# Kernel optimization log

Hardware: AMD Instinct MI355X
Metric: run time of the kernel (lower is better)

The kernel has to match this reference:

```python
import jax, jax.numpy as jnp
import numpy as np

B, C, T = 4, 512, 4096


def setup_inputs() -> dict:
    key = jax.random.key(0)
    ks = jax.random.split(key, 9)
    s = 1.0 / np.sqrt(C)
    return {
        "x": jax.random.normal(ks[0], (B, C, T), jnp.float32),
        "Wq": jax.random.normal(ks[1], (C, C), jnp.float32) * s,
        "bq": jax.random.normal(ks[2], (C,), jnp.float32) * 0.01,
        "Wk": jax.random.normal(ks[3], (C, C), jnp.float32) * s,
        "bk": jax.random.normal(ks[4], (C,), jnp.float32) * 0.01,
        "Wv": jax.random.normal(ks[5], (C, C), jnp.float32) * s,
        "bv": jax.random.normal(ks[6], (C,), jnp.float32) * 0.01,
        "Wp": jax.random.normal(ks[7], (C, C), jnp.float32) * s,
        "bp": jax.random.normal(ks[8], (C,), jnp.float32) * 0.01,
    }


def reference(x, Wq, bq, Wk, bk, Wv, bv, Wp, bp):
    # x: [B, C, T]; kernel-size-1 causal convs == pointwise linears over channels.
    b, c, t = x.shape
    q = jnp.einsum('oc,bct->bto', Wq, x) + bq  # [B, T, C]
    k = jnp.einsum('oc,bct->bto', Wk, x) + bk
    v = jnp.einsum('oc,bct->bto', Wv, x) + bv
    scale = jnp.asarray(c, x.dtype) ** -0.5
    w = jnp.einsum('btc,bsc->bts', q, k) * scale  # [B, T, T]
    mask = jnp.tril(jnp.ones((t, t), bool))        # causal: query t attends s<=t
    w = jnp.where(mask, w, -jnp.inf)
    w = jax.nn.softmax(w, axis=-1)
    h = jnp.einsum('bts,bsc->btc', w, v)           # [B, T, C]
    out = jnp.einsum('oc,btc->bot', Wp, h) + bp[None, :, None]  # [B, C, T]
    return x + out
```

## Files before the change

### kernel.cpp

```cpp
#include <hip/hip_runtime.h>

#define NB 4
#define NC 512
#define NT 4096
#define NTILE 528

typedef __attribute__((ext_vector_type(4))) float f32x4;
typedef __attribute__((ext_vector_type(8))) short short8;

typedef const __attribute__((address_space(1))) unsigned int* gp1_t;
typedef __attribute__((address_space(3))) unsigned int* lp3_t;

__device__ __forceinline__ void gload16(const short* g, short* l) {
  __builtin_amdgcn_global_load_lds((gp1_t)g, (lp3_t)l, 16, 0, 0);
}

#define BARRIER()  asm volatile("s_barrier" ::: "memory")
#define WAITVM0()  asm volatile("s_waitcnt vmcnt(0)" ::: "memory")
#define WAITVM4()  asm volatile("s_waitcnt vmcnt(4)" ::: "memory")
#define WAITVM8()  asm volatile("s_waitcnt vmcnt(8)" ::: "memory")
#define WAITVM12() asm volatile("s_waitcnt vmcnt(12)" ::: "memory")
#define WAITVM16() asm volatile("s_waitcnt vmcnt(16)" ::: "memory")

__device__ __forceinline__ short f2bf(float f) {
  union { float f; unsigned u; } v; v.f = f;
  unsigned r = v.u + 0x7fffu + ((v.u >> 16) & 1u);
  return (short)(r >> 16);
}
__device__ __forceinline__ float bf2f(short s) {
  union { unsigned u; float f; } v; v.u = ((unsigned)(unsigned short)s) << 16;
  return v.f;
}

#define SCOL_SWZ(lane) ((((lane) & 3) ^ (((lane) >> 3) & 3)) * 8)
#define FKO_SWZ(lane)  (((((lane) >> 4) ^ (((lane) >> 1) & 3)) & 3) * 8)

template <int NBUF>
__device__ __forceinline__ void gemm_tile(const short* __restrict__ A, int lda,
                                          const short* __restrict__ Bg, int ldb,
                                          int m0, int n0, int ksteps,
                                          f32x4 (&acc)[4][4], short* lds) {
  const int tid  = threadIdx.x;
  const int lane = tid & 63;
  const int wv   = tid >> 6;
  const int wm = (wv >> 1) * 64;
  const int wn = (wv & 1) * 64;
  const int srow = wv * 16 + (lane >> 2);
  const int scol = SCOL_SWZ(lane);
  const int fm  = lane & 15;
  const int fko = FKO_SWZ(lane);

  const short* Ap0 = A  + (size_t)(m0 + srow) * lda + scol;
  const short* Ap1 = Ap0 + (size_t)64 * lda;
  const short* Bp0 = Bg + (size_t)(n0 + srow) * ldb + scol;
  const short* Bp1 = Bp0 + (size_t)64 * ldb;

  auto issue = [&](int kt) {
    short* base = lds + (kt % NBUF) * 8192;
    const int k0 = kt * 32;
    gload16(Ap0 + k0, base + wv * 512);
    gload16(Ap1 + k0, base + 2048 + wv * 512);
    gload16(Bp0 + k0, base + 4096 + wv * 512);
    gload16(Bp1 + k0, base + 6144 + wv * 512);
  };

  issue(0);
#pragma unroll
  for (int p = 1; p < NBUF - 1; ++p)
    if (p < ksteps) issue(p);

  for (int kt = 0; kt < ksteps; ++kt) {
    const short* As = lds + (kt % NBUF) * 8192;
    const short* Bs = As + 4096;
    if (kt) BARRIER();
    if constexpr (NBUF == 5) {
      if (kt + 4 < ksteps)      { issue(kt + 4); WAITVM16(); }
      else if (kt + 3 < ksteps) { WAITVM12(); }
      else if (kt + 2 < ksteps) { WAITVM8(); }
      else if (kt + 1 < ksteps) { WAITVM4(); }
      else                      { WAITVM0(); }
    } else {
      if (kt + 2 < ksteps)      { issue(kt + 2); WAITVM8(); }
      else if (kt + 1 < ksteps) { WAITVM4(); }
      else                      { WAITVM0(); }
    }
    BARRIER();
    short8 af[4], bfr[4];
#pragma unroll
    for (int i = 0; i < 4; ++i)
      af[i] = *(const short8*)(As + (wm + i * 16 + fm) * 32 + fko);
#pragma unroll
    for (int j = 0; j < 4; ++j)
      bfr[j] = *(const short8*)(Bs + (wn + j * 16 + fm) * 32 + fko);
#pragma unroll
    for (int i = 0; i < 4; ++i)
#pragma unroll
      for (int j = 0; j < 4; ++j)
        acc[i][j] = __builtin_amdgcn_mfma_f32_16x16x32_bf16(af[i], bfr[j], acc[i][j], 0, 0, 0);
  }
}

#define ACC_INIT                                  \
  f32x4 acc[4][4];                                \
  {                                               \
    const f32x4 z = {0.f, 0.f, 0.f, 0.f};         \
    for (int i = 0; i < 4; ++i)                   \
      for (int j = 0; j < 4; ++j) acc[i][j] = z;  \
  }

#define EPI_IDX                                   \
  const int lane = threadIdx.x & 63;              \
  const int wave = threadIdx.x >> 6;              \
  const int wm = (wave >> 1) * 64;                \
  const int wn = (wave & 1) * 64;

#define GEMM_LDS3 __shared__ short lds[24576];
#define GEMM_LDS5 __shared__ short lds[40960];

__device__ __forceinline__ void xcd_rowchunk(int x, int nrows, int& row, int& chunk) {
  const int xcd  = x & 7;
  const int slot = x >> 3;
  row   = nrows - 1 - (xcd + 8 * (slot >> 2));
  chunk = slot & 3;
}

__device__ __forceinline__ void pv_rowchunk(int x, int z, int& bm, int& chunk) {
  const int xcd  = x & 7;
  const int slot = x >> 3;
  int ridx = slot >> 2;
  if (z >= 2) ridx = 3 - ridx;
  bm = (ridx == 0) ? (31 - xcd)
     : (ridx == 1) ? (23 - xcd)
     : (ridx == 2) ? (8 + xcd)
                   : xcd;
  chunk = slot & 3;
}

__global__ __launch_bounds__(256) void k_transpose(const float* __restrict__ x,
                                                   short* __restrict__ xT) {
  __shared__ float tile[32][33];
  const int b  = blockIdx.z;
  const int t0 = blockIdx.x * 32;
  const int c0 = blockIdx.y * 32;
  const int tx = threadIdx.x & 31;
  const int ty = threadIdx.x >> 5;
  const float* xp = x + ((size_t)b * NC + c0) * NT + t0;
#pragma unroll
  for (int i = 0; i < 32; i += 8)
    tile[ty + i][tx] = xp[(size_t)(ty + i) * NT + tx];
  __syncthreads();
  short* op = xT + ((size_t)b * NT + t0) * NC + c0;
#pragma unroll
  for (int i = 0; i < 32; i += 8)
    op[(size_t)(ty + i) * NC + tx] = f2bf(tile[tx][ty + i]);
}

__global__ __launch_bounds__(256) void k_wcvt(const float* __restrict__ s0, const float* __restrict__ s1,
                                              const float* __restrict__ s2, const float* __restrict__ s3,
                                              short* __restrict__ d0, short* __restrict__ d1,
                                              short* __restrict__ d2, short* __restrict__ d3) {
  const float* s; short* d;
  switch (blockIdx.y) {
    case 0: s = s0; d = d0; break;
    case 1: s = s1; d = d1; break;
    case 2: s = s2; d = d2; break;
    default: s = s3; d = d3; break;
  }
  const int i = (blockIdx.x * 256 + threadIdx.x) * 4;
  const float4 v = *(const float4*)(s + i);
  short4 o;
  o.x = f2bf(v.x); o.y = f2bf(v.y); o.z = f2bf(v.z); o.w = f2bf(v.w);
  *(short4*)(d + i) = o;
}

__global__ __launch_bounds__(256, 3) void k_qkv(const short* __restrict__ xT,
                                                const short* __restrict__ Wq,
                                                const float* __restrict__ bq,
                                                const short* __restrict__ Wk,
                                                const float* __restrict__ bk,
                                                const short* __restrict__ Wv,
                                                const float* __restrict__ bv,
                                                short* __restrict__ Q,
                                                short* __restrict__ K,
                                                short* __restrict__ VT) {
  GEMM_LDS3;
  const int b = blockIdx.z;
  const int y = blockIdx.y;
  int row, chunk;
  xcd_rowchunk((int)blockIdx.x, NT / 128, row, chunk);
  const short* Xb = xT + (size_t)b * NT * NC;
  ACC_INIT;
  if (y < 2) {
    const short* W = (y == 0) ? Wq : Wk;
    const float* bias = (y == 0) ? bq : bk;
    short* O = ((y == 0) ? Q : K) + (size_t)b * NT * NC;
    const int m0 = row * 128;
    const int n0 = chunk * 128;
    gemm_tile<3>(Xb, NC, W, NC, m0, n0, NC / 32, acc, lds);
    EPI_IDX;
#pragma unroll
    for (int j = 0; j < 4; ++j) {
      const int n = n0 + wn + j * 16 + (lane & 15);
      const float bv_ = bias[n];
#pragma unroll
      for (int i = 0; i < 4; ++i) {
        const int mb = m0 + wm + i * 16 + ((lane >> 4) * 4);
#pragma unroll
        for (int r = 0; r < 4; ++r)
          O[(size_t)(mb + r) * NC + n] = f2bf(acc[i][j][r] + bv_);
      }
    }
  } else {
    const int n0 = row * 128;
    const int m0 = chunk * 128;
    gemm_tile<3>(Wv, NC, Xb, NC, m0, n0, NC / 32, acc, lds);
    EPI_IDX;
    short* O = VT + (size_t)b * NC * NT;
#pragma unroll
    for (int j = 0; j < 4; ++j) {
      const int n = n0 + wn + j * 16 + (lane & 15);
#pragma unroll
      for (int i = 0; i < 4; ++i) {
        const int mb = m0 + wm + i * 16 + ((lane >> 4) * 4);
#pragma unroll
        for (int r = 0; r < 4; ++r)
          O[(size_t)(mb + r) * NT + n] = f2bf(acc[i][j][r] + bv[mb + r]);
      }
    }
  }
}

__global__ __launch_bounds__(256, 3) void k_scores(const short* __restrict__ Q,
                                                   const short* __restrict__ K,
                                                   short* __restrict__ P,
                                                   float* __restrict__ Lrow) {
  const int p = (((int)blockIdx.x & 7) * 66) + ((int)blockIdx.x >> 3);
  int bm = 0, bn = 0;
  {
    int base = 0;
    for (int sr = 0; sr < 4; ++sr) {
      bool done = false;
      for (int sc = 0; sc <= sr; ++sc) {
        const int sz = (sc == sr) ? 36 : 64;
        if (p < base + sz) {
          const int q = p - base;
          int i, j;
          if (sc == sr) {
            i = 0;
            while ((i + 1) * (i + 2) / 2 <= q) ++i;
            j = q - i * (i + 1) / 2;
          } else { i = q >> 3; j = q & 7; }
          bm = sr * 8 + i; bn = sc * 8 + j;
          done = true; break;
        }
        base += sz;
      }
      if (done) break;
    }
  }
  GEMM_LDS3;
  const int b  = blockIdx.z;
  const int m0 = bm * 128;
  const int n0 = bn * 128;
  ACC_INIT;
  gemm_tile<3>(Q + (size_t)b * NT * NC, NC, K + (size_t)b * NT * NC, NC,
               m0, n0, NC / 32, acc, lds);
  EPI_IDX;
  const float kls = 0.06376070265f;
  const int idx = bm * (bm + 1) / 2 + bn;
  short* Tp = P + ((size_t)b * NTILE + (size_t)idx) * 16384;
  float* Lp = Lrow + (size_t)b * NT;
  float psum[4][4];
#pragma unroll
  for (int i = 0; i < 4; ++i)
#pragma unroll
    for (int r = 0; r < 4; ++r) psum[i][r] = 0.f;

  if (bn < bm) {
#pragma unroll
    for (int j = 0; j < 4; ++j) {
      const int ln = wn + j * 16 + (lane & 15);
#pragma unroll
      for (int i = 0; i < 4; ++i) {
        const int lmb = wm + i * 16 + ((lane >> 4) * 4);
        const float e0 = exp2f(acc[i][j][0] * kls);
        const float e1 = exp2f(acc[i][j][1] * kls);
        const float e2 = exp2f(acc[i][j][2] * kls);
        const float e3 = exp2f(acc[i][j][3] * kls);
        unsigned pk01, pk23;
        asm("v_cvt_pk_bf16_f32 %0, %1, %2" : "=v"(pk01) : "v"(e0), "v"(e1));
        asm("v_cvt_pk_bf16_f32 %0, %1, %2" : "=v"(pk23) : "v"(e2), "v"(e3));
        Tp[(lmb + 0) * 128 + ln] = (short)(pk01 & 0xffffu);
        Tp[(lmb + 1) * 128 + ln] = (short)(pk01 >> 16);
        Tp[(lmb + 2) * 128 + ln] = (short)(pk23 & 0xffffu);
        Tp[(lmb + 3) * 128 + ln] = (short)(pk23 >> 16);
        union { unsigned u; float f; } c0, c1, c2, c3;
        c0.u = pk01 << 16; c1.u = pk01 & 0xffff0000u;
        c2.u = pk23 << 16; c3.u = pk23 & 0xffff0000u;
        psum[i][0] += c0.f; psum[i][1] += c1.f;
        psum[i][2] += c2.f; psum[i][3] += c3.f;
      }
    }
  } else {
#pragma unroll
    for (int j = 0; j < 4; ++j) {
      const int ln = wn + j * 16 + (lane & 15);
      const int n  = n0 + ln;
#pragma unroll
      for (int i = 0; i < 4; ++i) {
        const int lmb = wm + i * 16 + ((lane >> 4) * 4);
#pragma unroll
        for (int r = 0; r < 4; ++r) {
          const int m = m0 + lmb + r;
          float pr = 0.f;
          short pb = 0;
          if (n <= m) {
            pb = f2bf(exp2f(acc[i][j][r] * kls));
            pr = bf2f(pb);
          }
          Tp[(lmb + r) * 128 + ln] = pb;
          psum[i][r] += pr;
        }
      }
    }
  }
#pragma unroll
  for (int i = 0; i < 4; ++i)
#pragma unroll
    for (int r = 0; r < 4; ++r) {
      float v = psum[i][r];
      v += __shfl_xor(v, 1);
      v += __shfl_xor(v, 2);
      v += __shfl_xor(v, 4);
      v += __shfl_xor(v, 8);
      if ((lane & 15) == 0) {
        const int m = m0 + wm + i * 16 + ((lane >> 4) * 4) + r;
        atomicAdd(&Lp[m], v);
      }
    }
}

__global__ __launch_bounds__(256, 2) void k_pv(const short* __restrict__ P,
                                               const short* __restrict__ VT,
                                               const float* __restrict__ Lr,
                                               short* __restrict__ H) {
  GEMM_LDS5;
  const int b = blockIdx.z;
  int bm, chunk;
  pv_rowchunk((int)blockIdx.x, b, bm, chunk);
  const int m0 = bm * 128;
  const int n0 = chunk * 128;
  const int ksteps = (bm + 1) * 4;

  const short* Ptri = P + ((size_t)b * NTILE + (size_t)bm * (bm + 1) / 2) * 16384;
  const short* Bg   = VT + (size_t)b * NC * NT;

  ACC_INIT;
  const int tid  = threadIdx.x;
  const int lane = tid & 63;
  const int wv   = tid >> 6;
  const int wm = (wv >> 1) * 64;
  const int wn = (wv & 1) * 64;
  const int srow = wv * 16 + (lane >> 2);
  const int scol = SCOL_SWZ(lane);
  const int fm  = lane & 15;
  const int fko = FKO_SWZ(lane);

  const short* Bp0 = Bg + (size_t)(n0 + srow) * NT + scol;
  const short* Bp1 = Bp0 + (size_t)64 * NT;

  auto issue = [&](int kt) {
    short* base = lds + (kt % 5) * 8192;
    const short* At = Ptri + (size_t)(kt >> 2) * 16384 + (kt & 3) * 32;
    const short* Ap0 = At + srow * 128 + scol;
    const int k0 = kt * 32;
    gload16(Ap0, base + wv * 512);
    gload16(Ap0 + 64 * 128, base + 2048 + wv * 512);
    gload16(Bp0 + k0, base + 4096 + wv * 512);
    gload16(Bp1 + k0, base + 6144 + wv * 512);
  };

  issue(0);
#pragma unroll
  for (int p = 1; p < 4; ++p)
    if (p < ksteps) issue(p);
  for (int kt = 0; kt < ksteps; ++kt) {
    const short* As = lds + (kt % 5) * 8192;
    const short* Bs = As + 4096;
    if (kt) BARRIER();
    if (kt + 4 < ksteps)      { issue(kt + 4); WAITVM16(); }
    else if (kt + 3 < ksteps) { WAITVM12(); }
    else if (kt + 2 < ksteps) { WAITVM8(); }
    else if (kt + 1 < ksteps) { WAITVM4(); }
    else                      { WAITVM0(); }
    BARRIER();
    short8 af[4], bfr[4];
#pragma unroll
    for (int i = 0; i < 4; ++i)
      af[i] = *(const short8*)(As + (wm + i * 16 + fm) * 32 + fko);
#pragma unroll
    for (int j = 0; j < 4; ++j)
      bfr[j] = *(const short8*)(Bs + (wn + j * 16 + fm) * 32 + fko);
#pragma unroll
    for (int i = 0; i < 4; ++i)
#pragma unroll
      for (int j = 0; j < 4; ++j)
        acc[i][j] = __builtin_amdgcn_mfma_f32_16x16x32_bf16(af[i], bfr[j], acc[i][j], 0, 0, 0);
  }

  const float* L = Lr + (size_t)b * NT;
  short* Hp = H + (size_t)b * NT * NC;
#pragma unroll
  for (int i = 0; i < 4; ++i) {
    const int mb = m0 + wm + i * 16 + ((lane >> 4) * 4);
    float rinv[4];
#pragma unroll
    for (int r = 0; r < 4; ++r) rinv[r] = 1.f / L[mb + r];
#pragma unroll
    for (int j = 0; j < 4; ++j) {
      const int n = n0 + wn + j * 16 + (lane & 15);
#pragma unroll
      for (int r = 0; r < 4; ++r)
        Hp[(size_t)(mb + r) * NC + n] = f2bf(acc[i][j][r] * rinv[r]);
    }
  }
}

__global__ __launch_bounds__(256, 2) void k_out(const short* __restrict__ W,
                                                const short* __restrict__ H,
                                                const float* __restrict__ bias,
                                                const float* __restrict__ x,
                                                float* __restrict__ out) {
  GEMM_LDS5;
  const int b = blockIdx.z;
  int row, chunk;
  xcd_rowchunk((int)blockIdx.x, NT / 128, row, chunk);
  const int n0 = row * 128;
  const int m0 = chunk * 128;
  ACC_INIT;
  gemm_tile<5>(W, NC, H + (size_t)b * NT * NC, NC, m0, n0, NC / 32, acc, lds);
  EPI_IDX;
#pragma unroll
  for (int j = 0; j < 4; ++j) {
    const int n = n0 + wn + j * 16 + (lane & 15);
#pragma unroll
    for (int i = 0; i < 4; ++i) {
      const int mb = m0 + wm + i * 16 + ((lane >> 4) * 4);
#pragma unroll
      for (int r = 0; r < 4; ++r) {
        const int m = mb + r;
        const size_t idx = ((size_t)b * NC + m) * NT + n;
        out[idx] = acc[i][j][r] + bias[m] + x[idx];
      }
    }
  }
}

extern "C" void kernel_launch(void* const* d_in, const int* in_sizes, int n_in,
                              void* d_out, int out_size, void* d_ws, size_t ws_size,
                              hipStream_t stream) {
  (void)in_sizes; (void)n_in; (void)out_size; (void)ws_size;
  const float* x  = (const float*)d_in[0];
  const float* Wq = (const float*)d_in[1];
  const float* bq = (const float*)d_in[2];
  const float* Wk = (const float*)d_in[3];
  const float* bk = (const float*)d_in[4];
  const float* Wv = (const float*)d_in[5];
  const float* bv = (const float*)d_in[6];
  const float* Wp = (const float*)d_in[7];
  const float* bp = (const float*)d_in[8];
  float* out = (float*)d_out;

  char* ws = (char*)d_ws;
  size_t off = 0;
  auto alloc = [&](size_t bytes) { char* p = ws + off; off += bytes; return p; };
  short* xT  = (short*)alloc((size_t)NB * NT * NC * 2);
  short* Qb  = (short*)alloc((size_t)NB * NT * NC * 2);
  short* Kb  = (short*)alloc((size_t)NB * NT * NC * 2);
  short* VTb = (short*)alloc((size_t)NB * NC * NT * 2);
  short* Hb  = (short*)alloc((size_t)NB * NT * NC * 2);
  short* Wqb = (short*)alloc((size_t)NC * NC * 2);
  short* Wkb = (short*)alloc((size_t)NC * NC * 2);
  short* Wvb = (short*)alloc((size_t)NC * NC * 2);
  short* Wpb = (short*)alloc((size_t)NC * NC * 2);
  float* Lr  = (float*)alloc((size_t)NB * NT * 4);
  short* Pb  = (short*)alloc((size_t)NB * NTILE * 16384 * 2);

  hipMemsetAsync(Lr, 0, (size_t)NB * NT * 4, stream);

  const dim3 blk(256);
  k_wcvt<<<dim3(NC * NC / 1024, 4), blk, 0, stream>>>(Wq, Wk, Wv, Wp, Wqb, Wkb, Wvb, Wpb);

  k_transpose<<<dim3(NT / 32, NC / 32, NB), blk, 0, stream>>>(x, xT);

  k_qkv<<<dim3(128, 3, NB), blk, 0, stream>>>(xT, Wqb, bq, Wkb, bk, Wvb, bv, Qb, Kb, VTb);

  k_scores<<<dim3(NTILE, 1, NB), blk, 0, stream>>>(Qb, Kb, Pb, Lr);
  k_pv<<<dim3(128, 1, NB), blk, 0, stream>>>(Pb, VTb, Lr, Hb);
  k_out<<<dim3(128, 1, NB), blk, 0, stream>>>(Wpb, Hb, bp, x, out);
}
```

Measured before the change: 273.0 us.

## Use 128x256 GEMM tiles for QKV projection and causal score kernels

Adds a gemm_tile256 routine where each block computes a 128x256 output tile, with waves covering 64x128 sub-tiles, and switches k_qkv and k_scores to it. The score kernel now covers pairs of 128-column key blocks per launch and remaps the triangular tile enumeration so that 272 blocks per batch replace 528. Each wave exits early if its half lies above the diagonal. The aim is more operand reuse per LDS load and fewer blocks. The cost is more accumulator registers, more LDS, lower occupancy (launch bounds 3 down to 2), and idle waves in diagonal tiles.

Result: no change. 273.8 us (+0.3%).

```diff
diff --git a/kernel.cpp b/kernel.cpp
--- a/kernel.cpp
+++ b/kernel.cpp
@@ -18,6 +18,7 @@
 #define BARRIER()  asm volatile("s_barrier" ::: "memory")
 #define WAITVM0()  asm volatile("s_waitcnt vmcnt(0)" ::: "memory")
 #define WAITVM4()  asm volatile("s_waitcnt vmcnt(4)" ::: "memory")
+#define WAITVM6()  asm volatile("s_waitcnt vmcnt(6)" ::: "memory")
 #define WAITVM8()  asm volatile("s_waitcnt vmcnt(8)" ::: "memory")
 #define WAITVM12() asm volatile("s_waitcnt vmcnt(12)" ::: "memory")
 #define WAITVM16() asm volatile("s_waitcnt vmcnt(16)" ::: "memory")
@@ -100,6 +101,63 @@
   }
 }
 
+__device__ __forceinline__ void gemm_tile256(const short* __restrict__ A, int lda,
+                                             const short* __restrict__ Bg, int ldb,
+                                             int m0, int n0, int ksteps,
+                                             f32x4 (&acc)[4][8], short* lds) {
+  const int tid  = threadIdx.x;
+  const int lane = tid & 63;
+  const int wv   = tid >> 6;
+  const int wm = (wv >> 1) * 64;
+  const int wn = (wv & 1) * 128;
+  const int srow = wv * 16 + (lane >> 2);
+  const int scol = SCOL_SWZ(lane);
+  const int fm  = lane & 15;
+  const int fko = FKO_SWZ(lane);
+
+  const short* Ap0 = A  + (size_t)(m0 + srow) * lda + scol;
+  const short* Ap1 = Ap0 + (size_t)64 * lda;
+  const short* Bp0 = Bg + (size_t)(n0 + srow) * ldb + scol;
+  const short* Bp1 = Bp0 + (size_t)64 * ldb;
+  const short* Bp2 = Bp0 + (size_t)128 * ldb;
+  const short* Bp3 = Bp0 + (size_t)192 * ldb;
+
+  auto issue = [&](int kt) {
+    short* base = lds + (kt % 3) * 12288;
+    const int k0 = kt * 32;
+    gload16(Ap0 + k0, base + wv * 512);
+    gload16(Ap1 + k0, base + 2048 + wv * 512);
+    gload16(Bp0 + k0, base + 4096 + wv * 512);
+    gload16(Bp1 + k0, base + 6144 + wv * 512);
+    gload16(Bp2 + k0, base + 8192 + wv * 512);
+    gload16(Bp3 + k0, base + 10240 + wv * 512);
+  };
+
+  issue(0);
+  if (ksteps > 1) issue(1);
+  for (int kt = 0; kt < ksteps; ++kt) {
+    const short* As = lds + (kt % 3) * 12288;
+    const short* Bs = As + 4096;
+    if (kt) BARRIER();
+    if (kt + 2 < ksteps)      { issue(kt + 2); WAITVM12(); }
+    else if (kt + 1 < ksteps) { WAITVM6(); }
+    else                      { WAITVM0(); }
+    BARRIER();
+    short8 af[4], bfr[8];
+#pragma unroll
+    for (int i = 0; i < 4; ++i)
+      af[i] = *(const short8*)(As + (wm + i * 16 + fm) * 32 + fko);
+#pragma unroll
+    for (int j = 0; j < 8; ++j)
+      bfr[j] = *(const short8*)(Bs + (wn + j * 16 + fm) * 32 + fko);
+#pragma unroll
+    for (int i = 0; i < 4; ++i)
+#pragma unroll
+      for (int j = 0; j < 8; ++j)
+        acc[i][j] = __builtin_amdgcn_mfma_f32_16x16x32_bf16(af[i], bfr[j], acc[i][j], 0, 0, 0);
+  }
+}
+
 #define ACC_INIT                                  \
   f32x4 acc[4][4];                                \
   {                                               \
@@ -108,14 +166,28 @@
       for (int j = 0; j < 4; ++j) acc[i][j] = z;  \
   }
 
+#define ACC_INIT256                               \
+  f32x4 acc[4][8];                                \
+  {                                               \
+    const f32x4 z = {0.f, 0.f, 0.f, 0.f};         \
+    for (int i = 0; i < 4; ++i)                   \
+      for (int j = 0; j < 8; ++j) acc[i][j] = z;  \
+  }
+
 #define EPI_IDX                                   \
   const int lane = threadIdx.x & 63;              \
   const int wave = threadIdx.x >> 6;              \
   const int wm = (wave >> 1) * 64;                \
   const int wn = (wave & 1) * 64;
 
-#define GEMM_LDS3 __shared__ short lds[24576];
-#define GEMM_LDS5 __shared__ short lds[40960];
+#define EPI_IDX256                                \
+  const int lane = threadIdx.x & 63;              \
+  const int wave = threadIdx.x >> 6;              \
+  const int wm = (wave >> 1) * 64;                \
+  const int wn = (wave & 1) * 128;
+
+#define GEMM_LDS256 __shared__ short lds[36864];
+#define GEMM_LDS5   __shared__ short lds[40960];
 
 __device__ __forceinline__ void xcd_rowchunk(int x, int nrows, int& row, int& chunk) {
   const int xcd  = x & 7;
@@ -173,7 +245,7 @@
   *(short4*)(d + i) = o;
 }
 
-__global__ __launch_bounds__(256, 3) void k_qkv(const short* __restrict__ xT,
+__global__ __launch_bounds__(256, 2) void k_qkv(const short* __restrict__ xT,
                                                 const short* __restrict__ Wq,
                                                 const float* __restrict__ bq,
                                                 const short* __restrict__ Wk,
@@ -183,23 +255,23 @@
                                                 short* __restrict__ Q,
                                                 short* __restrict__ K,
                                                 short* __restrict__ VT) {
-  GEMM_LDS3;
+  GEMM_LDS256;
   const int b = blockIdx.z;
   const int y = blockIdx.y;
-  int row, chunk;
-  xcd_rowchunk((int)blockIdx.x, NT / 128, row, chunk);
+  const int x = blockIdx.x;
+  const int sw = (x & 7) * 8 + (x >> 3);
   const short* Xb = xT + (size_t)b * NT * NC;
-  ACC_INIT;
+  ACC_INIT256;
   if (y < 2) {
     const short* W = (y == 0) ? Wq : Wk;
     const float* bias = (y == 0) ? bq : bk;
     short* O = ((y == 0) ? Q : K) + (size_t)b * NT * NC;
-    const int m0 = row * 128;
-    const int n0 = chunk * 128;
-    gemm_tile<3>(Xb, NC, W, NC, m0, n0, NC / 32, acc, lds);
-    EPI_IDX;
-#pragma unroll
-    for (int j = 0; j < 4; ++j) {
+    const int m0 = (sw >> 1) * 128;
+    const int n0 = (sw & 1) * 256;
+    gemm_tile256(Xb, NC, W, NC, m0, n0, NC / 32, acc, lds);
+    EPI_IDX256;
+#pragma unroll
+    for (int j = 0; j < 8; ++j) {
       const int n = n0 + wn + j * 16 + (lane & 15);
       const float bv_ = bias[n];
 #pragma unroll
@@ -211,13 +283,13 @@
       }
     }
   } else {
-    const int n0 = row * 128;
-    const int m0 = chunk * 128;
-    gemm_tile<3>(Wv, NC, Xb, NC, m0, n0, NC / 32, acc, lds);
-    EPI_IDX;
+    const int m0 = (sw & 3) * 128;
+    const int n0 = (sw >> 2) * 256;
+    gemm_tile256(Wv, NC, Xb, NC, m0, n0, NC / 32, acc, lds);
+    EPI_IDX256;
     short* O = VT + (size_t)b * NC * NT;
 #pragma unroll
-    for (int j = 0; j < 4; ++j) {
+    for (int j = 0; j < 8; ++j) {
       const int n = n0 + wn + j * 16 + (lane & 15);
 #pragma unroll
       for (int i = 0; i < 4; ++i) {
@@ -230,45 +302,36 @@
   }
 }
 
-__global__ __launch_bounds__(256, 3) void k_scores(const short* __restrict__ Q,
+__global__ __launch_bounds__(256, 2) void k_scores(const short* __restrict__ Q,
                                                    const short* __restrict__ K,
                                                    short* __restrict__ P,
                                                    float* __restrict__ Lrow) {
-  const int p = (((int)blockIdx.x & 7) * 66) + ((int)blockIdx.x >> 3);
-  int bm = 0, bn = 0;
-  {
-    int base = 0;
-    for (int sr = 0; sr < 4; ++sr) {
-      bool done = false;
-      for (int sc = 0; sc <= sr; ++sc) {
-        const int sz = (sc == sr) ? 36 : 64;
-        if (p < base + sz) {
-          const int q = p - base;
-          int i, j;
-          if (sc == sr) {
-            i = 0;
-            while ((i + 1) * (i + 2) / 2 <= q) ++i;
-            j = q - i * (i + 1) / 2;
-          } else { i = q >> 3; j = q & 7; }
-          bm = sr * 8 + i; bn = sc * 8 + j;
-          done = true; break;
-        }
-        base += sz;
-      }
-      if (done) break;
-    }
-  }
-  GEMM_LDS3;
+  const int x = blockIdx.x;
+  const int p = (x & 7) * 34 + (x >> 3);
+  int bm = 0, pk = 0;
+#pragma unroll
+  for (int a = 0; a < 16; ++a) {
+    const int e0 = a * (a + 1);
+    const int e1 = (a + 1) * (a + 1);
+    const int e2 = (a + 1) * (a + 2);
+    if (p < e1) { bm = 2 * a; pk = p - e0; break; }
+    if (p < e2) { bm = 2 * a + 1; pk = p - e1; break; }
+  }
+  GEMM_LDS256;
   const int b  = blockIdx.z;
   const int m0 = bm * 128;
-  const int n0 = bn * 128;
-  ACC_INIT;
-  gemm_tile<3>(Q + (size_t)b * NT * NC, NC, K + (size_t)b * NT * NC, NC,
+  const int n0 = pk * 256;
+  ACC_INIT256;
+  gemm_tile256(Q + (size_t)b * NT * NC, NC, K + (size_t)b * NT * NC, NC,
                m0, n0, NC / 32, acc, lds);
-  EPI_IDX;
+  const int lane = threadIdx.x & 63;
+  const int wave = threadIdx.x >> 6;
+  const int wm = (wave >> 1) * 64;
+  const int half = wave & 1;
+  const int bn = 2 * pk + half;
+  if (bn > bm) return;
   const float kls = 0.06376070265f;
-  const int idx = bm * (bm + 1) / 2 + bn;
-  short* Tp = P + ((size_t)b * NTILE + (size_t)idx) * 16384;
+  short* Tp = P + ((size_t)b * NTILE + (size_t)(bm * (bm + 1) / 2 + bn)) * 16384;
   float* Lp = Lrow + (size_t)b * NT;
   float psum[4][4];
 #pragma unroll
@@ -278,8 +341,8 @@
 
   if (bn < bm) {
 #pragma unroll
-    for (int j = 0; j < 4; ++j) {
-      const int ln = wn + j * 16 + (lane & 15);
+    for (int j = 0; j < 8; ++j) {
+      const int ln = j * 16 + (lane & 15);
 #pragma unroll
       for (int i = 0; i < 4; ++i) {
         const int lmb = wm + i * 16 + ((lane >> 4) * 4);
@@ -303,9 +366,9 @@
     }
   } else {
 #pragma unroll
-    for (int j = 0; j < 4; ++j) {
-      const int ln = wn + j * 16 + (lane & 15);
-      const int n  = n0 + ln;
+    for (int j = 0; j < 8; ++j) {
+      const int ln = j * 16 + (lane & 15);
+      const int n  = bn * 128 + ln;
 #pragma unroll
       for (int i = 0; i < 4; ++i) {
         const int lmb = wm + i * 16 + ((lane >> 4) * 4);
@@ -493,9 +556,9 @@
 
   k_transpose<<<dim3(NT / 32, NC / 32, NB), blk, 0, stream>>>(x, xT);
 
-  k_qkv<<<dim3(128, 3, NB), blk, 0, stream>>>(xT, Wqb, bq, Wkb, bk, Wvb, bv, Qb, Kb, VTb);
-
-  k_scores<<<dim3(NTILE, 1, NB), blk, 0, stream>>>(Qb, Kb, Pb, Lr);
+  k_qkv<<<dim3(64, 3, NB), blk, 0, stream>>>(xT, Wqb, bq, Wkb, bk, Wvb, bv, Qb, Kb, VTb);
+
+  k_scores<<<dim3(272, 1, NB), blk, 0, stream>>>(Qb, Kb, Pb, Lr);
   k_pv<<<dim3(128, 1, NB), blk, 0, stream>>>(Pb, VTb, Lr, Hb);
   k_out<<<dim3(128, 1, NB), blk, 0, stream>>>(Wpb, Hb, bp, x, out);
 }
```
